# Optimization experiments

Hardware: AMD Instinct MI355X
Metric: run time of the kernel (lower is better)

Reference implementation:

```python
import jax, jax.numpy as jnp
import numpy as np

B, T = 4096, 16384

def setup_inputs() -> dict:
    key = jax.random.key(0)
    ks = jax.random.split(key, 6)
    x = jax.random.normal(ks[0], (B, T), dtype=jnp.float32)
    v0 = jnp.zeros((B, 2), dtype=jnp.float32)
    # match torch init ranges: b* ~ U(-1,1), a* ~ U(-0.5,0.5) (stable region)
    b0 = jax.random.uniform(ks[1], (1,), jnp.float32, -1.0, 1.0)
    b1 = jax.random.uniform(ks[2], (1,), jnp.float32, -1.0, 1.0)
    b2 = jax.random.uniform(ks[3], (1,), jnp.float32, -1.0, 1.0)
    a1 = jax.random.uniform(ks[4], (1,), jnp.float32, -0.5, 0.5)
    a2 = jax.random.uniform(ks[5], (1,), jnp.float32, -0.5, 0.5)
    return {"x": x, "v0": v0, "b0": b0, "b1": b1, "b2": b2, "a1": a1, "a2": a2}

def reference(x, v0, b0, b1, b2, a1, a2):
    """DF-II transposed biquad, scanned over time.
    x: [B, T] input samples; v0: [B, 2] initial state.
    Returns (y [B, T], v_final [B, 2]).
    Per-step math is exactly DTDFIICell.forward:
      y   = x_t * b0 + v[:,0]
      v0' = x_t * b1 + v[:,1] - y * a1
      v1' = x_t * b2            - y * a2
    """
    def step(v, xt):  # v: [B,2], xt: [B]
        y = xt * b0 + v[:, 0]                      # [B]
        v_new = jnp.stack(
            [xt * b1 + v[:, 1] - y * a1,
             xt * b2 - y * a2], axis=-1)           # [B,2]
        return v_new, y
    v_final, ys = jax.lax.scan(step, v0, x.T)      # ys: [T, B]
    return ys.T, v_final
```

## Files before the change

### kernel.cpp

```cpp
#include <hip/hip_runtime.h>

#define B_DIM 4096
#define T_DIM 16384
#define WAVES_PER_BLOCK 4
#define PER_LANE 8
#define CHUNK (64 * PER_LANE)

typedef float f32x4 __attribute__((ext_vector_type(4)));

struct M2 { float a, b, c, d; };

__device__ inline M2 m2mul(const M2& X, const M2& Y) {
    M2 r;
    r.a = fmaf(X.a, Y.a, X.b * Y.c);
    r.b = fmaf(X.a, Y.b, X.b * Y.d);
    r.c = fmaf(X.c, Y.a, X.d * Y.c);
    r.d = fmaf(X.c, Y.b, X.d * Y.d);
    return r;
}

__global__ __launch_bounds__(256, 4) void biquad_scan_kernel(
    const float* __restrict__ x, const float* __restrict__ v0in,
    const float* __restrict__ pb0, const float* __restrict__ pb1,
    const float* __restrict__ pb2, const float* __restrict__ pa1,
    const float* __restrict__ pa2,
    float* __restrict__ y, float* __restrict__ vout)
{
    const int lane = threadIdx.x & 63;
    const int wave = threadIdx.x >> 6;
    const int row  = blockIdx.x * WAVES_PER_BLOCK + wave;
    if (row >= B_DIM) return;

    const float b0 = *pb0, b1 = *pb1, b2 = *pb2, a1 = *pa1, a2 = *pa2;
    const float na1 = -a1, na2 = -a2;
    const float c0 = b1 - a1 * b0;
    const float c1 = b2 - a2 * b0;

    M2 A  { na1, 1.0f, na2, 0.0f };
    M2 A2 = m2mul(A, A);
    M2 A3 = m2mul(A2, A);
    M2 A4 = m2mul(A2, A2);
    M2 A5 = m2mul(A4, A);
    M2 A6 = m2mul(A4, A2);
    M2 A7 = m2mul(A4, A3);
    M2 A8 = m2mul(A4, A4);

    const float p1a = A .a, p1b = A .b;
    const float p2a = A2.a, p2b = A2.b;
    const float p3a = A3.a, p3b = A3.b;
    const float p4a = A4.a, p4b = A4.b;
    const float p5a = A5.a, p5b = A5.b;
    const float p6a = A6.a, p6b = A6.b;
    const float p7a = A7.a, p7b = A7.b;

    M2 S0, S1, S2, S3, S4, S5;
    M2 Q { 1.f, 0.f, 0.f, 1.f };
    M2 M = A8;
    S0 = M; if (lane & 1)  Q = m2mul(M, Q); M = m2mul(M, M);
    S1 = M; if (lane & 2)  Q = m2mul(M, Q); M = m2mul(M, M);
    S2 = M; if (lane & 4)  Q = m2mul(M, Q); M = m2mul(M, M);
    S3 = M; if (lane & 8)  Q = m2mul(M, Q); M = m2mul(M, M);
    S4 = M; if (lane & 16) Q = m2mul(M, Q); M = m2mul(M, M);
    S5 = M; if (lane & 32) Q = m2mul(M, Q); M = m2mul(M, M);
    const M2 R = M;

    const float* xr = x + (size_t)row * T_DIM;
    float*       yr = y + (size_t)row * T_DIM;

    float vc0 = v0in[row * 2 + 0];
    float vc1 = v0in[row * 2 + 1];

    const int NIT = T_DIM / CHUNK;
    const int STEP4 = CHUNK / 4;

    const f32x4* xp = (const f32x4*)xr + lane * 2;
    f32x4*       yp = (f32x4*)yr + lane * 2;

    f32x4 ca = __builtin_nontemporal_load(&xp[0]);
    f32x4 cb = __builtin_nontemporal_load(&xp[1]);
    xp += STEP4;
    f32x4 pa = __builtin_nontemporal_load(&xp[0]);
    f32x4 pb = __builtin_nontemporal_load(&xp[1]);

    for (int i = 0; i < NIT; ++i) {
        f32x4 ma = {0.f, 0.f, 0.f, 0.f}, mb = {0.f, 0.f, 0.f, 0.f};
        if (i + 2 < NIT) {
            ma = __builtin_nontemporal_load(&xp[STEP4]);
            mb = __builtin_nontemporal_load(&xp[STEP4 + 1]);
        }

        float d0 = 0.f, d1 = 0.f;
        float yz0, yz1, yz2, yz3, yz4, yz5, yz6, yz7;
        #define FOLD(xs, yz)                                           \
        {   yz = fmaf((xs), b0, d0);                                   \
            float t0 = fmaf(c0, (xs), fmaf(na1, d0, d1));              \
            float t1 = fmaf(na2, d0, c1 * (xs));                       \
            d0 = t0; d1 = t1; }
        FOLD(ca[0], yz0) FOLD(ca[1], yz1) FOLD(ca[2], yz2) FOLD(ca[3], yz3)
        FOLD(cb[0], yz4) FOLD(cb[1], yz5) FOLD(cb[2], yz6) FOLD(cb[3], yz7)
        #undef FOLD

        #define SCAN_STEP(Sm, o)                                        \
        {   float q0 = __shfl_up(d0, (unsigned)(o));                    \
            float q1 = __shfl_up(d1, (unsigned)(o));                    \
            if (lane < (o)) { q0 = 0.f; q1 = 0.f; }                     \
            float t0 = fmaf(Sm.a, q0, fmaf(Sm.b, q1, d0));              \
            float t1 = fmaf(Sm.c, q0, fmaf(Sm.d, q1, d1));              \
            d0 = t0; d1 = t1; }
        SCAN_STEP(S0, 1)
        SCAN_STEP(S1, 2)
        SCAN_STEP(S2, 4)
        SCAN_STEP(S3, 8)
        SCAN_STEP(S4, 16)
        SCAN_STEP(S5, 32)
        #undef SCAN_STEP

        float e0 = __shfl_up(d0, 1u);
        float e1 = __shfl_up(d1, 1u);
        if (lane == 0) { e0 = 0.f; e1 = 0.f; }

        const float vb0 = fmaf(Q.a, vc0, fmaf(Q.b, vc1, e0));
        const float vb1 = fmaf(Q.c, vc0, fmaf(Q.d, vc1, e1));

        f32x4 yo0, yo1;
        yo0[0] = yz0 + vb0;
        yo0[1] = fmaf(p1a, vb0, fmaf(p1b, vb1, yz1));
        yo0[2] = fmaf(p2a, vb0, fmaf(p2b, vb1, yz2));
        yo0[3] = fmaf(p3a, vb0, fmaf(p3b, vb1, yz3));
        yo1[0] = fmaf(p4a, vb0, fmaf(p4b, vb1, yz4));
        yo1[1] = fmaf(p5a, vb0, fmaf(p5b, vb1, yz5));
        yo1[2] = fmaf(p6a, vb0, fmaf(p6b, vb1, yz6));
        yo1[3] = fmaf(p7a, vb0, fmaf(p7b, vb1, yz7));

        __builtin_nontemporal_store(yo0, &yp[0]);
        __builtin_nontemporal_store(yo1, &yp[1]);

        float t0 = __shfl(d0, 63);
        float t1 = __shfl(d1, 63);
        float nv0 = fmaf(R.a, vc0, fmaf(R.b, vc1, t0));
        float nv1 = fmaf(R.c, vc0, fmaf(R.d, vc1, t1));
        vc0 = nv0; vc1 = nv1;

        ca = pa; cb = pb; pa = ma; pb = mb;
        xp += STEP4;
        yp += STEP4;
    }

    if (lane == 0) {
        vout[row * 2 + 0] = vc0;
        vout[row * 2 + 1] = vc1;
    }
}

extern "C" void kernel_launch(void* const* d_in, const int* in_sizes, int n_in,
                              void* d_out, int out_size, void* d_ws, size_t ws_size,
                              hipStream_t stream) {
    const float* x   = (const float*)d_in[0];
    const float* v0  = (const float*)d_in[1];
    const float* b0  = (const float*)d_in[2];
    const float* b1  = (const float*)d_in[3];
    const float* b2  = (const float*)d_in[4];
    const float* a1  = (const float*)d_in[5];
    const float* a2  = (const float*)d_in[6];

    float* y    = (float*)d_out;
    float* vout = (float*)d_out + (size_t)B_DIM * T_DIM;

    dim3 grid(B_DIM / WAVES_PER_BLOCK);
    dim3 block(64 * WAVES_PER_BLOCK);
    biquad_scan_kernel<<<grid, block, 0, stream>>>(x, v0, b0, b1, b2, a1, a2, y, vout);
}
```

Before: 124.9 us.

## Shrink per-lane chunk to 4 samples and deepen load prefetch to four iterations

Each lane now handles 4 samples per iteration instead of 8, giving 256-sample chunks and twice as many scan iterations per row. The two-deep nontemporal prefetch becomes a four-deep register rotation using plain loads and stores, and the occupancy hint is dropped from launch bounds. The aim is more loads in flight and fewer registers per lane to hide memory latency. The cost is doubling the per-chunk shuffle scan and carry work relative to the samples processed, and losing the nontemporal cache hints.

```diff
diff --git a/kernel.cpp b/kernel.cpp
--- a/kernel.cpp
+++ b/kernel.cpp
@@ -3,8 +3,8 @@
 #define B_DIM 4096
 #define T_DIM 16384
 #define WAVES_PER_BLOCK 4
-#define PER_LANE 8
-#define CHUNK (64 * PER_LANE)
+#define CHUNK 256
+#define NIT (T_DIM / CHUNK)
 
 typedef float f32x4 __attribute__((ext_vector_type(4)));
 
@@ -19,7 +19,7 @@
     return r;
 }
 
-__global__ __launch_bounds__(256, 4) void biquad_scan_kernel(
+__global__ __launch_bounds__(256) void biquad_scan_kernel(
     const float* __restrict__ x, const float* __restrict__ v0in,
     const float* __restrict__ pb0, const float* __restrict__ pb1,
     const float* __restrict__ pb2, const float* __restrict__ pa1,
@@ -40,22 +40,14 @@
     M2 A2 = m2mul(A, A);
     M2 A3 = m2mul(A2, A);
     M2 A4 = m2mul(A2, A2);
-    M2 A5 = m2mul(A4, A);
-    M2 A6 = m2mul(A4, A2);
-    M2 A7 = m2mul(A4, A3);
-    M2 A8 = m2mul(A4, A4);
 
     const float p1a = A .a, p1b = A .b;
     const float p2a = A2.a, p2b = A2.b;
     const float p3a = A3.a, p3b = A3.b;
-    const float p4a = A4.a, p4b = A4.b;
-    const float p5a = A5.a, p5b = A5.b;
-    const float p6a = A6.a, p6b = A6.b;
-    const float p7a = A7.a, p7b = A7.b;
 
     M2 S0, S1, S2, S3, S4, S5;
     M2 Q { 1.f, 0.f, 0.f, 1.f };
-    M2 M = A8;
+    M2 M = A4;
     S0 = M; if (lane & 1)  Q = m2mul(M, Q); M = m2mul(M, M);
     S1 = M; if (lane & 2)  Q = m2mul(M, Q); M = m2mul(M, M);
     S2 = M; if (lane & 4)  Q = m2mul(M, Q); M = m2mul(M, M);
@@ -70,34 +62,30 @@
     float vc0 = v0in[row * 2 + 0];
     float vc1 = v0in[row * 2 + 1];
 
-    const int NIT = T_DIM / CHUNK;
-    const int STEP4 = CHUNK / 4;
+    const int S4STEP = CHUNK / 4;
+    const f32x4* xp = (const f32x4*)xr + lane;
+    f32x4*       yp = (f32x4*)yr + lane;
 
-    const f32x4* xp = (const f32x4*)xr + lane * 2;
-    f32x4*       yp = (f32x4*)yr + lane * 2;
+    f32x4 r0 = xp[0 * S4STEP];
+    f32x4 r1 = xp[1 * S4STEP];
+    f32x4 r2 = xp[2 * S4STEP];
+    f32x4 r3 = xp[3 * S4STEP];
 
-    f32x4 ca = __builtin_nontemporal_load(&xp[0]);
-    f32x4 cb = __builtin_nontemporal_load(&xp[1]);
-    xp += STEP4;
-    f32x4 pa = __builtin_nontemporal_load(&xp[0]);
-    f32x4 pb = __builtin_nontemporal_load(&xp[1]);
-
+    #pragma unroll 4
     for (int i = 0; i < NIT; ++i) {
-        f32x4 ma = {0.f, 0.f, 0.f, 0.f}, mb = {0.f, 0.f, 0.f, 0.f};
-        if (i + 2 < NIT) {
-            ma = __builtin_nontemporal_load(&xp[STEP4]);
-            mb = __builtin_nontemporal_load(&xp[STEP4 + 1]);
-        }
+        const f32x4 xv = r0;
+        r0 = r1; r1 = r2; r2 = r3;
+        int nf = i + 4; if (nf > NIT - 1) nf = NIT - 1;
+        r3 = xp[(size_t)nf * S4STEP];
 
         float d0 = 0.f, d1 = 0.f;
-        float yz0, yz1, yz2, yz3, yz4, yz5, yz6, yz7;
+        float yz0, yz1, yz2, yz3;
         #define FOLD(xs, yz)                                           \
         {   yz = fmaf((xs), b0, d0);                                   \
             float t0 = fmaf(c0, (xs), fmaf(na1, d0, d1));              \
             float t1 = fmaf(na2, d0, c1 * (xs));                       \
             d0 = t0; d1 = t1; }
-        FOLD(ca[0], yz0) FOLD(ca[1], yz1) FOLD(ca[2], yz2) FOLD(ca[3], yz3)
-        FOLD(cb[0], yz4) FOLD(cb[1], yz5) FOLD(cb[2], yz6) FOLD(cb[3], yz7)
+        FOLD(xv[0], yz0) FOLD(xv[1], yz1) FOLD(xv[2], yz2) FOLD(xv[3], yz3)
         #undef FOLD
 
         #define SCAN_STEP(Sm, o)                                        \
@@ -122,28 +110,19 @@
         const float vb0 = fmaf(Q.a, vc0, fmaf(Q.b, vc1, e0));
         const float vb1 = fmaf(Q.c, vc0, fmaf(Q.d, vc1, e1));
 
-        f32x4 yo0, yo1;
-        yo0[0] = yz0 + vb0;
-        yo0[1] = fmaf(p1a, vb0, fmaf(p1b, vb1, yz1));
-        yo0[2] = fmaf(p2a, vb0, fmaf(p2b, vb1, yz2));
-        yo0[3] = fmaf(p3a, vb0, fmaf(p3b, vb1, yz3));
-        yo1[0] = fmaf(p4a, vb0, fmaf(p4b, vb1, yz4));
-        yo1[1] = fmaf(p5a, vb0, fmaf(p5b, vb1, yz5));
-        yo1[2] = fmaf(p6a, vb0, fmaf(p6b, vb1, yz6));
-        yo1[3] = fmaf(p7a, vb0, fmaf(p7b, vb1, yz7));
+        f32x4 yo;
+        yo[0] = yz0 + vb0;
+        yo[1] = fmaf(p1a, vb0, fmaf(p1b, vb1, yz1));
+        yo[2] = fmaf(p2a, vb0, fmaf(p2b, vb1, yz2));
+        yo[3] = fmaf(p3a, vb0, fmaf(p3b, vb1, yz3));
 
-        __builtin_nontemporal_store(yo0, &yp[0]);
-        __builtin_nontemporal_store(yo1, &yp[1]);
+        yp[(size_t)i * S4STEP] = yo;
 
         float t0 = __shfl(d0, 63);
         float t1 = __shfl(d1, 63);
         float nv0 = fmaf(R.a, vc0, fmaf(R.b, vc1, t0));
         float nv1 = fmaf(R.c, vc0, fmaf(R.d, vc1, t1));
         vc0 = nv0; vc1 = nv1;
-
-        ca = pa; cb = pb; pa = ma; pb = mb;
-        xp += STEP4;
-        yp += STEP4;
     }
 
     if (lane == 0) {
```

After: 119.1 us. 4.6% less time.
